# Optimization experiments

Hardware: AMD Instinct MI355X
Metric: run time of the kernel (lower is better)

The kernel has to match this reference:

```python
import jax, jax.numpy as jnp
import numpy as np

V = 33279   # num_tokens
E = 256     # embedding_size
H = 512     # hidden_size
NH = 8      # num_heads
L = 4       # num_layers
DH = E // NH
MAXPOS = 64


def _ln(x, g, b):
    mu = jnp.mean(x, axis=-1, keepdims=True)
    var = jnp.mean((x - mu) ** 2, axis=-1, keepdims=True)
    return (x - mu) / jnp.sqrt(var + 1e-5) * g + b


def setup_inputs() -> dict:
    key = jax.random.key(0)
    ks = jax.random.split(key, 32)
    N, S = 128, 64
    label = jax.random.randint(ks[0], (N, S), 0, V)
    # Bernoulli(0.15) BERT-style mask (deterministic stand-in for torch sampling)
    mask = (jax.random.uniform(ks[1], (N, S)) < 0.15).astype(jnp.int32)
    s = 0.02
    inp = {
        'label': label, 'mask': mask,
        'emb': jax.random.normal(ks[2], (V + 1, E)) * s,
        'pos': jax.random.normal(ks[3], (MAXPOS, E)) * s,
        'emb_g': jnp.ones((E,)), 'emb_b': jnp.zeros((E,)),
        # stacked per-layer params (leading dim L)
        'Wq': jax.random.normal(ks[4], (L, E, E)) * s, 'bq': jnp.zeros((L, E)),
        'Wk': jax.random.normal(ks[5], (L, E, E)) * s, 'bk': jnp.zeros((L, E)),
        'Wv': jax.random.normal(ks[6], (L, E, E)) * s, 'bv': jnp.zeros((L, E)),
        'Wo': jax.random.normal(ks[7], (L, E, E)) * s, 'bo': jnp.zeros((L, E)),
        'n1g': jnp.ones((L, E)), 'n1b': jnp.zeros((L, E)),
        'W1': jax.random.normal(ks[8], (L, E, H)) * s, 'b1': jnp.zeros((L, H)),
        'W2': jax.random.normal(ks[9], (L, H, E)) * s, 'b2': jnp.zeros((L, E)),
        'n2g': jnp.ones((L, E)), 'n2b': jnp.zeros((L, E)),
        # decoder head
        'dW1': jax.random.normal(ks[10], (E, E)) * s, 'db1': jnp.zeros((E,)),
        'dng': jnp.ones((E,)), 'dnb': jnp.zeros((E,)),
        'dW2': jax.random.normal(ks[11], (E, V)) * s, 'db2': jnp.zeros((V,)),
    }
    return inp


def reference(label, mask, emb, pos, emb_g, emb_b, Wq, bq, Wk, bk, Wv, bv,
              Wo, bo, n1g, n1b, W1, b1, W2, b2, n2g, n2b,
              dW1, db1, dng, dnb, dW2, db2):
    N, S = label.shape
    src_ids = jnp.where(mask == 1, V, label)  # masked-token id = num_tokens
    # embedding + positional, then LayerNorm (eval: Scaler/Dropout identity)
    x = emb[src_ids] + pos[:S][None, :, :]
    x = _ln(x, emb_g, emb_b)
    temp = jnp.asarray((E // NH) ** 0.5, x.dtype)

    def layer(x, p):
        wq, bq_, wk, bk_, wv, bv_, wo, bo_, g1, b1n, w1, b1_, w2, b2_, g2, b2n = p
        q = (x @ wq + bq_).reshape(N, S, NH, DH).transpose(0, 2, 1, 3)
        k = (x @ wk + bk_).reshape(N, S, NH, DH).transpose(0, 2, 1, 3)
        v = (x @ wv + bv_).reshape(N, S, NH, DH).transpose(0, 2, 1, 3)
        scores = jnp.einsum('nhsd,nhtd->nhst', q, k) / temp
        attn = jax.nn.softmax(scores, axis=-1)
        o = jnp.einsum('nhst,nhtd->nhsd', attn, v)
        o = o.transpose(0, 2, 1, 3).reshape(N, S, E) @ wo + bo_
        x1 = _ln(x + o, g1, b1n)
        ff = jax.nn.gelu(x1 @ w1 + b1_, approximate=False) @ w2 + b2_
        x2 = _ln(x1 + ff, g2, b2n)
        return x2, None

    x, _ = jax.lax.scan(layer, x, (Wq, bq, Wk, bk, Wv, bv, Wo, bo,
                                   n1g, n1b, W1, b1, W2, b2, n2g, n2b))
    # decoder head: linear -> gelu -> LN -> vocab projection
    h = jax.nn.gelu(x @ dW1 + db1, approximate=False)
    h = _ln(h, dng, dnb)
    logits = h @ dW2 + db2               # [N, S, V]
    logp = jax.nn.log_softmax(logits, axis=-1)
    loss = -jnp.take_along_axis(logp, label[..., None], axis=-1).mean()
    score = logits.transpose(0, 2, 1)    # [N, V, S] like torch permute(0,2,1)
    return score, loss
```

## Files before the change

kernel.cpp:

```cpp
#include <hip/hip_runtime.h>
#include <hip/hip_bf16.h>

#define DEVFN static __device__ __forceinline__

constexpr int N_ = 128, S_ = 64, T_ = N_ * S_;
constexpr int E_ = 256, H_ = 512, NH_ = 8, DH_ = 32, L_ = 4;
constexpr int V_ = 33279, VPAD_ = 33280, NVT_ = VPAD_ / 256;

typedef __attribute__((ext_vector_type(8))) short bf16x8;
typedef __attribute__((ext_vector_type(4))) float f32x4;
typedef unsigned short ushort_t;

DEVFN ushort_t f2bf(float f) {
  unsigned int u = __float_as_uint(f);
  unsigned int r = (u + 0x7fffu + ((u >> 16) & 1u)) >> 16;
  return (ushort_t)r;
}
DEVFN float bf2f(ushort_t u) { return __uint_as_float(((unsigned)u) << 16); }

DEVFN float geluf(float x) {
  return 0.5f * x * (1.f + erff(x * 0.70710678118654752440f));
}

DEVFN float wave_sum(float v) {
  #pragma unroll
  for (int off = 32; off >= 1; off >>= 1) v += __shfl_xor(v, off, 64);
  return v;
}

DEVFN float l15_sum(float v) {
  v += __shfl_xor(v, 1, 64);
  v += __shfl_xor(v, 2, 64);
  v += __shfl_xor(v, 4, 64);
  v += __shfl_xor(v, 8, 64);
  return v;
}

__global__ __launch_bounds__(256) void k_embed_ln(
    const int* __restrict__ label, const int* __restrict__ mask,
    const float* __restrict__ emb, const float* __restrict__ pos,
    const float* __restrict__ g, const float* __restrict__ b,
    float* __restrict__ x, ushort_t* __restrict__ xb) {
  int wv = threadIdx.x >> 6, lane = threadIdx.x & 63;
  int t = blockIdx.x * 4 + wv;
  int s = t & (S_ - 1);
  int id = (mask[t] == 1) ? V_ : label[t];
  int c = lane * 4;
  float4 v = *(const float4*)&emb[(size_t)id * E_ + c];
  float4 p = *(const float4*)&pos[s * E_ + c];
  v.x += p.x; v.y += p.y; v.z += p.z; v.w += p.w;
  float mean = wave_sum(v.x + v.y + v.z + v.w) * (1.f / E_);
  float4 d = {v.x - mean, v.y - mean, v.z - mean, v.w - mean};
  float var = wave_sum(d.x * d.x + d.y * d.y + d.z * d.z + d.w * d.w) * (1.f / E_);
  float rstd = 1.f / sqrtf(var + 1e-5f);
  float4 g4 = *(const float4*)&g[c];
  float4 b4 = *(const float4*)&b[c];
  float4 y = {d.x * rstd * g4.x + b4.x, d.y * rstd * g4.y + b4.y,
              d.z * rstd * g4.z + b4.z, d.w * rstd * g4.w + b4.w};
  *(float4*)&x[(size_t)t * E_ + c] = y;
  ushort4 yb = {f2bf(y.x), f2bf(y.y), f2bf(y.z), f2bf(y.w)};
  *(ushort4*)&xb[(size_t)t * E_ + c] = yb;
}

__global__ __launch_bounds__(256) void k_bcat(
    const float* __restrict__ bq, const float* __restrict__ bk,
    const float* __restrict__ bv, float* __restrict__ bqkv) {
  int l = blockIdx.x, i = threadIdx.x;
  bqkv[l * 768 + i]       = bq[l * 256 + i];
  bqkv[l * 768 + 256 + i] = bk[l * 256 + i];
  bqkv[l * 768 + 512 + i] = bv[l * 256 + i];
}

__global__ __launch_bounds__(256) void k_wt(const float* __restrict__ src,
                                            ushort_t* __restrict__ dst,
                                            int K, int J, int dstLayerStride) {
  __shared__ float tile[32][33];
  int j0 = blockIdx.x * 32, k0 = blockIdx.y * 32, l = blockIdx.z;
  src += (size_t)l * K * J;
  dst += (size_t)l * dstLayerStride;
  int tx = threadIdx.x & 31, ty = threadIdx.x >> 5;
  #pragma unroll
  for (int rr = 0; rr < 4; rr++) {
    int kk = ty * 4 + rr;
    tile[kk][tx] = src[(size_t)(k0 + kk) * J + j0 + tx];
  }
  __syncthreads();
  #pragma unroll
  for (int rr = 0; rr < 4; rr++) {
    int jj = ty * 4 + rr;
    dst[(size_t)(j0 + jj) * K + k0 + tx] = f2bf(tile[tx][jj]);
  }
}

__global__ __launch_bounds__(256) void k_wtE(
    const float* __restrict__ Wq, const float* __restrict__ Wk,
    const float* __restrict__ Wv, const float* __restrict__ Wo,
    const float* __restrict__ dW1, ushort_t* __restrict__ wqkvT,
    ushort_t* __restrict__ woT, ushort_t* __restrict__ dw1T) {
  __shared__ float tile[32][33];
  int z = blockIdx.z;
  const float* src;
  ushort_t* dst;
  if (z == 4 * L_) {
    src = dW1; dst = dw1T;
  } else {
    int w = z >> 2, l = z & 3;
    const float* ws = (w == 0) ? Wq : (w == 1) ? Wk : (w == 2) ? Wv : Wo;
    src = ws + (size_t)l * E_ * E_;
    dst = (w < 3) ? (wqkvT + (size_t)l * 768 * E_ + (size_t)w * 256 * E_)
                  : (woT + (size_t)l * E_ * E_);
  }
  int j0 = blockIdx.x * 32, k0 = blockIdx.y * 32;
  int tx = threadIdx.x & 31, ty = threadIdx.x >> 5;
  #pragma unroll
  for (int rr = 0; rr < 4; rr++) {
    int kk = ty * 4 + rr;
    tile[kk][tx] = src[(size_t)(k0 + kk) * E_ + j0 + tx];
  }
  __syncthreads();
  #pragma unroll
  for (int rr = 0; rr < 4; rr++) {
    int jj = ty * 4 + rr;
    dst[(size_t)(j0 + jj) * E_ + k0 + tx] = f2bf(tile[tx][jj]);
  }
}

template <int K, int OUT_BF16, int GELU_>
__global__ __launch_bounds__(256) void k_mm(
    const ushort_t* __restrict__ Xb, const ushort_t* __restrict__ WT,
    const float* __restrict__ bias, void* __restrict__ C, int Nout) {
  constexpr int STR = K + 8;
  __shared__ ushort_t xs[64 * STR];
  int tid = threadIdx.x, lane = tid & 63, wv = tid >> 6;
  int t0 = blockIdx.x * 64, j0 = blockIdx.y * 64;
  const ushort_t* xsrc = Xb + (size_t)t0 * K;
  for (int i = tid; i < 64 * (K / 8); i += 256) {
    int r = i / (K / 8), c = (i % (K / 8)) * 8;
    *(uint4*)&xs[r * STR + c] = *(const uint4*)&xsrc[(size_t)r * K + c];
  }
  __syncthreads();
  int l15 = lane & 15, l4 = lane >> 4;
  f32x4 acc[4] = {};
  const ushort_t* xrow = &xs[(wv * 16 + l15) * STR + l4 * 8];
  const ushort_t* wrow = WT + (size_t)j0 * K + l4 * 8;
  #pragma unroll
  for (int kb = 0; kb < K / 32; kb++) {
    bf16x8 a = *(const bf16x8*)(xrow + kb * 32);
    #pragma unroll
    for (int st = 0; st < 4; st++) {
      bf16x8 bfr = *(const bf16x8*)(wrow + (size_t)(st * 16 + l15) * K + kb * 32);
      acc[st] = __builtin_amdgcn_mfma_f32_16x16x32_bf16(a, bfr, acc[st], 0, 0, 0);
    }
  }
  #pragma unroll
  for (int st = 0; st < 4; st++) {
    int j = j0 + st * 16 + l15;
    float bv_ = bias[j];
    #pragma unroll
    for (int r = 0; r < 4; r++) {
      float val = acc[st][r] + bv_;
      if (GELU_) val = geluf(val);
      int t = t0 + wv * 16 + l4 * 4 + r;
      if (OUT_BF16)
        ((ushort_t*)C)[(size_t)t * Nout + j] = f2bf(val);
      else
        ((float*)C)[(size_t)t * Nout + j] = val;
    }
  }
}

template <int K, int GELU_PRE, int HAS_RES, int OUT_F32>
__global__ __launch_bounds__(256) void k_mm_ln2(
    const ushort_t* __restrict__ Xb, const ushort_t* __restrict__ WT,
    const float* __restrict__ bias, const float* __restrict__ res,
    const float* __restrict__ g, const float* __restrict__ bet,
    float* __restrict__ y, ushort_t* __restrict__ yb) {
  constexpr int STR = K + 8;
  __shared__ ushort_t xs[16 * STR];
  __shared__ float redA[4][16], redB[4][16];
  int tid = threadIdx.x, lane = tid & 63, wv = tid >> 6;
  int t0 = blockIdx.x * 16;
  const ushort_t* xsrc = Xb + (size_t)t0 * K;
  for (int i = tid; i < 16 * (K / 8); i += 256) {
    int r = i / (K / 8), c = (i % (K / 8)) * 8;
    *(uint4*)&xs[r * STR + c] = *(const uint4*)&xsrc[(size_t)r * K + c];
  }
  __syncthreads();
  int l15 = lane & 15, l4 = lane >> 4;
  f32x4 acc[4] = {};
  const ushort_t* xrow = &xs[l15 * STR + l4 * 8];
  const ushort_t* wrow = WT + (size_t)(wv * 64) * K + l4 * 8;
  #pragma unroll
  for (int kb = 0; kb < K / 32; kb++) {
    bf16x8 a = *(const bf16x8*)(xrow + kb * 32);
    #pragma unroll
    for (int st = 0; st < 4; st++) {
      bf16x8 bfr = *(const bf16x8*)(wrow + (size_t)(st * 16 + l15) * K + kb * 32);
      acc[st] = __builtin_amdgcn_mfma_f32_16x16x32_bf16(a, bfr, acc[st], 0, 0, 0);
    }
  }
  float val[4][4];
  #pragma unroll
  for (int st = 0; st < 4; st++) {
    int j = wv * 64 + st * 16 + l15;
    float bv_ = bias[j];
    #pragma unroll
    for (int r = 0; r < 4; r++) {
      float v = acc[st][r] + bv_;
      if (GELU_PRE) v = geluf(v);
      if (HAS_RES) v += res[(size_t)(t0 + l4 * 4 + r) * E_ + j];
      val[st][r] = v;
    }
  }
  #pragma unroll
  for (int r = 0; r < 4; r++) {
    float s = val[0][r] + val[1][r] + val[2][r] + val[3][r];
    s = l15_sum(s);
    if (l15 == 0) redA[wv][l4 * 4 + r] = s;
  }
  __syncthreads();
  float mean[4];
  #pragma unroll
  for (int r = 0; r < 4; r++) {
    int row = l4 * 4 + r;
    mean[r] = (redA[0][row] + redA[1][row] + redA[2][row] + redA[3][row]) * (1.f / E_);
  }
  #pragma unroll
  for (int r = 0; r < 4; r++) {
    float s = 0.f;
    #pragma unroll
    for (int st = 0; st < 4; st++) {
      float d = val[st][r] - mean[r];
      s += d * d;
    }
    s = l15_sum(s);
    if (l15 == 0) redB[wv][l4 * 4 + r] = s;
  }
  __syncthreads();
  float rstd[4];
  #pragma unroll
  for (int r = 0; r < 4; r++) {
    int row = l4 * 4 + r;
    float var = (redB[0][row] + redB[1][row] + redB[2][row] + redB[3][row]) * (1.f / E_);
    rstd[r] = 1.f / sqrtf(var + 1e-5f);
  }
  #pragma unroll
  for (int st = 0; st < 4; st++) {
    int j = wv * 64 + st * 16 + l15;
    float gj = g[j], bj = bet[j];
    #pragma unroll
    for (int r = 0; r < 4; r++) {
      int t = t0 + l4 * 4 + r;
      float o = (val[st][r] - mean[r]) * rstd[r] * gj + bj;
      if (OUT_F32) y[(size_t)t * E_ + j] = o;
      yb[(size_t)t * E_ + j] = f2bf(o);
    }
  }
}

__global__ __launch_bounds__(256) void k_attn(
    const ushort_t* __restrict__ qkv, ushort_t* __restrict__ o) {
  __shared__ __align__(16) ushort_t vt_[32 * 72];
  __shared__ __align__(16) ushort_t ps[64 * 72];
  int n = blockIdx.x >> 3, h = blockIdx.x & 7;
  int tid = threadIdx.x, lane = tid & 63, wv = tid >> 6;
  int l15 = lane & 15, l4 = lane >> 4;
  const ushort_t* qbase = qkv + (size_t)n * S_ * 768 + h * DH_;
  for (int i = tid; i < S_ * DH_; i += 256) {
    int t = i >> 5, d = i & 31;
    vt_[d * 72 + t] = qbase[(size_t)t * 768 + 512 + d];
  }
  int srow = wv * 16 + l15;
  bf16x8 aq = *(const bf16x8*)&qbase[(size_t)srow * 768 + l4 * 8];
  f32x4 sc[4];
  #pragma unroll
  for (int st = 0; st < 4; st++) {
    bf16x8 bk_ = *(const bf16x8*)&qbase[(size_t)(st * 16 + l15) * 768 + 256 + l4 * 8];
    f32x4 z = {};
    sc[st] = __builtin_amdgcn_mfma_f32_16x16x32_bf16(aq, bk_, z, 0, 0, 0);
  }
  const float scale = 0.17677669529663687f;
  #pragma unroll
  for (int st = 0; st < 4; st++)
    #pragma unroll
    for (int r = 0; r < 4; r++) sc[st][r] *= scale;
  #pragma unroll
  for (int r = 0; r < 4; r++) {
    float m = fmaxf(fmaxf(sc[0][r], sc[1][r]), fmaxf(sc[2][r], sc[3][r]));
    m = fmaxf(m, __shfl_xor(m, 1, 64));
    m = fmaxf(m, __shfl_xor(m, 2, 64));
    m = fmaxf(m, __shfl_xor(m, 4, 64));
    m = fmaxf(m, __shfl_xor(m, 8, 64));
    float p0 = __expf(sc[0][r] - m), p1 = __expf(sc[1][r] - m);
    float p2 = __expf(sc[2][r] - m), p3 = __expf(sc[3][r] - m);
    float sum = p0 + p1 + p2 + p3;
    sum += __shfl_xor(sum, 1, 64);
    sum += __shfl_xor(sum, 2, 64);
    sum += __shfl_xor(sum, 4, 64);
    sum += __shfl_xor(sum, 8, 64);
    float inv = 1.f / sum;
    int prow = (wv * 16 + l4 * 4 + r) * 72;
    ps[prow + 0 * 16 + l15] = f2bf(p0 * inv);
    ps[prow + 1 * 16 + l15] = f2bf(p1 * inv);
    ps[prow + 2 * 16 + l15] = f2bf(p2 * inv);
    ps[prow + 3 * 16 + l15] = f2bf(p3 * inv);
  }
  __syncthreads();
  f32x4 oc[2] = {};
  #pragma unroll
  for (int kb = 0; kb < 2; kb++) {
    bf16x8 ap = *(const bf16x8*)&ps[srow * 72 + kb * 32 + l4 * 8];
    #pragma unroll
    for (int st2 = 0; st2 < 2; st2++) {
      bf16x8 bv_ = *(const bf16x8*)&vt_[(st2 * 16 + l15) * 72 + kb * 32 + l4 * 8];
      oc[st2] = __builtin_amdgcn_mfma_f32_16x16x32_bf16(ap, bv_, oc[st2], 0, 0, 0);
    }
  }
  ushort_t* ob = o + (size_t)n * S_ * E_ + h * DH_;
  #pragma unroll
  for (int st2 = 0; st2 < 2; st2++)
    #pragma unroll
    for (int r = 0; r < 4; r++)
      ob[(size_t)(wv * 16 + l4 * 4 + r) * E_ + st2 * 16 + l15] = f2bf(oc[st2][r]);
}

__global__ __launch_bounds__(256) void k_w2t(const float* __restrict__ w,
                                             ushort_t* __restrict__ wt) {
  __shared__ float tile[32 * 33];
  int tx = threadIdx.x & 31, ty = threadIdx.x >> 5;
  int v0 = blockIdx.x * 32, k0 = blockIdx.y * 32;
  #pragma unroll
  for (int rr = 0; rr < 4; rr++) {
    int kk = ty * 4 + rr;
    int vv = v0 + tx;
    tile[kk * 33 + tx] = (vv < V_) ? w[(size_t)(k0 + kk) * V_ + vv] : 0.f;
  }
  __syncthreads();
  #pragma unroll
  for (int rr = 0; rr < 4; rr++) {
    int vv = ty * 4 + rr;
    wt[(size_t)(v0 + vv) * E_ + k0 + tx] = f2bf(tile[tx * 33 + vv]);
  }
}

__global__ __launch_bounds__(256) void k_vocab(
    const ushort_t* __restrict__ hbf, const ushort_t* __restrict__ wt,
    const float* __restrict__ db2, float* __restrict__ out,
    float* __restrict__ pmax, float* __restrict__ psum) {
  __shared__ ushort_t hs[64 * 264];
  __shared__ float redm[4][64];
  __shared__ float reds[4][64];
  int n = blockIdx.x, vt = blockIdx.y;
  int tid = threadIdx.x, lane = tid & 63, wv = tid >> 6;
  const ushort_t* hsrc = hbf + (size_t)n * S_ * E_;
  for (int i = tid; i < (S_ * E_) / 8; i += 256) {
    int s = i >> 5, kc = (i & 31) * 8;
    *(uint4*)&hs[s * 264 + kc] = *(const uint4*)&hsrc[s * E_ + kc];
  }
  __syncthreads();
  int l15 = lane & 15, l4 = lane >> 4;
  float rm[4], rs[4];
  #pragma unroll
  for (int st = 0; st < 4; st++) { rm[st] = -INFINITY; rs[st] = 0.f; }
  #pragma unroll
  for (int h2 = 0; h2 < 2; h2++) {
    const ushort_t* Ap0 =
        wt + (size_t)(vt * 256 + h2 * 128 + wv * 16 + l15) * E_ + l4 * 8;
    const ushort_t* Ap1 = Ap0 + (size_t)64 * E_;
    f32x4 acc[2][4] = {};
    #pragma unroll
    for (int kb = 0; kb < 8; kb++) {
      bf16x8 a0 = *(const bf16x8*)(Ap0 + kb * 32);
      bf16x8 a1 = *(const bf16x8*)(Ap1 + kb * 32);
      #pragma unroll
      for (int st = 0; st < 4; st++) {
        bf16x8 bfr = *(const bf16x8*)&hs[(st * 16 + l15) * 264 + kb * 32 + l4 * 8];
        acc[0][st] = __builtin_amdgcn_mfma_f32_16x16x32_bf16(a0, bfr, acc[0][st], 0, 0, 0);
        acc[1][st] = __builtin_amdgcn_mfma_f32_16x16x32_bf16(a1, bfr, acc[1][st], 0, 0, 0);
      }
    }
    float vals[2][4][4];
    #pragma unroll
    for (int mt = 0; mt < 2; mt++) {
      #pragma unroll
      for (int j = 0; j < 4; j++) {
        int v = vt * 256 + h2 * 128 + wv * 16 + mt * 64 + l4 * 4 + j;
        bool valid = v < V_;
        float bias = valid ? db2[v] : 0.f;
        size_t ob = ((size_t)n * V_ + v) * S_;
        #pragma unroll
        for (int st = 0; st < 4; st++) {
          float val = valid ? (acc[mt][st][j] + bias) : -INFINITY;
          vals[mt][st][j] = val;
          if (valid) __builtin_nontemporal_store(val, &out[ob + st * 16 + l15]);
        }
      }
    }
    #pragma unroll
    for (int st = 0; st < 4; st++) {
      float m = -INFINITY;
      #pragma unroll
      for (int mt = 0; mt < 2; mt++)
        #pragma unroll
        for (int j = 0; j < 4; j++) m = fmaxf(m, vals[mt][st][j]);
      m = fmaxf(m, __shfl_xor(m, 16, 64));
      m = fmaxf(m, __shfl_xor(m, 32, 64));
      float sum = 0.f;
      #pragma unroll
      for (int mt = 0; mt < 2; mt++)
        #pragma unroll
        for (int j = 0; j < 4; j++) sum += __expf(vals[mt][st][j] - m);
      sum += __shfl_xor(sum, 16, 64);
      sum += __shfl_xor(sum, 32, 64);
      float nm = fmaxf(rm[st], m);
      rs[st] = rs[st] * __expf(rm[st] - nm) + sum * __expf(m - nm);
      rm[st] = nm;
    }
  }
  if (l4 == 0) {
    #pragma unroll
    for (int st = 0; st < 4; st++) {
      redm[wv][st * 16 + l15] = rm[st];
      reds[wv][st * 16 + l15] = rs[st];
    }
  }
  __syncthreads();
  if (wv == 0 && l4 == 0) {
    #pragma unroll
    for (int st = 0; st < 4; st++) {
      int s = st * 16 + l15;
      float M = fmaxf(fmaxf(redm[0][s], redm[1][s]), fmaxf(redm[2][s], redm[3][s]));
      float Sa = reds[0][s] * __expf(redm[0][s] - M) +
                 reds[1][s] * __expf(redm[1][s] - M) +
                 reds[2][s] * __expf(redm[2][s] - M) +
                 reds[3][s] * __expf(redm[3][s] - M);
      size_t pi = ((size_t)n * NVT_ + vt) * S_ + s;
      pmax[pi] = M;
      psum[pi] = Sa;
    }
  }
}

__global__ __launch_bounds__(512) void k_lossf(
    const float* __restrict__ pmax, const float* __restrict__ psum,
    const float* __restrict__ out, const int* __restrict__ label,
    float* __restrict__ partial) {
  __shared__ float sm[512], ssum[512];
  int n = blockIdx.x, tid = threadIdx.x;
  int s = tid & 63, qq = tid >> 6;
  float m = -INFINITY, sum = 0.f;
  for (int vt = qq; vt < NVT_; vt += 8) {
    size_t pi = ((size_t)n * NVT_ + vt) * S_ + s;
    float m2 = pmax[pi], s2 = psum[pi];
    float nm = fmaxf(m, m2);
    sum = sum * __expf(m - nm) + s2 * __expf(m2 - nm);
    m = nm;
  }
  sm[tid] = m; ssum[tid] = sum;
  __syncthreads();
  if (qq == 0) {
    float M = sm[s], Sa = ssum[s];
    #pragma unroll
    for (int p = 1; p < 8; p++) {
      float m2 = sm[p * 64 + s], s2 = ssum[p * 64 + s];
      float nm = fmaxf(M, m2);
      Sa = Sa * __expf(M - nm) + s2 * __expf(m2 - nm);
      M = nm;
    }
    float lse = M + logf(Sa);
    int lab = label[n * S_ + s];
    float lx = out[((size_t)n * V_ + lab) * S_ + s];
    partial[n * S_ + s] = lse - lx;
  }
}

__global__ __launch_bounds__(256) void k_loss2(const float* __restrict__ partial,
                                               float* __restrict__ dst) {
  __shared__ float sbuf[4];
  int tid = threadIdx.x;
  float acc = 0.f;
  for (int i = tid; i < T_; i += 256) acc += partial[i];
  #pragma unroll
  for (int off = 32; off >= 1; off >>= 1) acc += __shfl_xor(acc, off, 64);
  int lane = tid & 63, wid = tid >> 6;
  if (lane == 0) sbuf[wid] = acc;
  __syncthreads();
  if (tid == 0) dst[0] = (sbuf[0] + sbuf[1] + sbuf[2] + sbuf[3]) / (float)T_;
}

extern "C" void kernel_launch(void* const* d_in, const int* in_sizes, int n_in,
                              void* d_out, int out_size, void* d_ws, size_t ws_size,
                              hipStream_t stream) {
  const int*   label = (const int*)d_in[0];
  const int*   mask  = (const int*)d_in[1];
  const float* emb   = (const float*)d_in[2];
  const float* pos   = (const float*)d_in[3];
  const float* emb_g = (const float*)d_in[4];
  const float* emb_b = (const float*)d_in[5];
  const float* Wq  = (const float*)d_in[6];
  const float* bq  = (const float*)d_in[7];
  const float* Wk  = (const float*)d_in[8];
  const float* bk  = (const float*)d_in[9];
  const float* Wv  = (const float*)d_in[10];
  const float* bv  = (const float*)d_in[11];
  const float* Wo  = (const float*)d_in[12];
  const float* bo  = (const float*)d_in[13];
  const float* n1g = (const float*)d_in[14];
  const float* n1b = (const float*)d_in[15];
  const float* W1  = (const float*)d_in[16];
  const float* b1  = (const float*)d_in[17];
  const float* W2  = (const float*)d_in[18];
  const float* b2  = (const float*)d_in[19];
  const float* n2g = (const float*)d_in[20];
  const float* n2b = (const float*)d_in[21];
  const float* dW1 = (const float*)d_in[22];
  const float* db1 = (const float*)d_in[23];
  const float* dng = (const float*)d_in[24];
  const float* dnb = (const float*)d_in[25];
  const float* dW2 = (const float*)d_in[26];
  const float* db2 = (const float*)d_in[27];
  float* out = (float*)d_out;
  (void)in_sizes; (void)n_in; (void)out_size; (void)ws_size;

  char* base = (char*)d_ws;
  size_t off = 0;
  auto alloc = [&](size_t bytes) {
    char* p = base + off;
    off += (bytes + 255) & ~(size_t)255;
    return p;
  };
  float*    x    = (float*)alloc((size_t)T_ * E_ * 4);
  ushort_t* xb   = (ushort_t*)alloc((size_t)T_ * E_ * 2);
  float*    x1   = (float*)alloc((size_t)T_ * E_ * 4);
  ushort_t* x1b  = (ushort_t*)alloc((size_t)T_ * E_ * 2);
  ushort_t* qkv  = (ushort_t*)alloc((size_t)T_ * 768 * 2);
  ushort_t* obuf = (ushort_t*)alloc((size_t)T_ * E_ * 2);
  ushort_t* wqkvT = (ushort_t*)alloc((size_t)L_ * 768 * E_ * 2);
  ushort_t* woT   = (ushort_t*)alloc((size_t)L_ * E_ * E_ * 2);
  ushort_t* w1T   = (ushort_t*)alloc((size_t)L_ * H_ * E_ * 2);
  ushort_t* w2T   = (ushort_t*)alloc((size_t)L_ * E_ * H_ * 2);
  ushort_t* dw1T  = (ushort_t*)alloc((size_t)E_ * E_ * 2);
  ushort_t* wt    = (ushort_t*)alloc((size_t)VPAD_ * E_ * 2);
  float*    bqkv  = (float*)alloc((size_t)L_ * 768 * 4);
  float*    partial = (float*)alloc((size_t)T_ * 4);
  ushort_t* ffh = qkv;
  ushort_t* hbf = obuf;
  float* pmax = x;
  float* psum = pmax + (size_t)N_ * NVT_ * S_;

  k_bcat<<<L_, 256, 0, stream>>>(bq, bk, bv, bqkv);
  k_wtE<<<dim3(8, 8, 4 * L_ + 1), 256, 0, stream>>>(Wq, Wk, Wv, Wo, dW1, wqkvT, woT, dw1T);
  k_wt<<<dim3(16, 8, L_), 256, 0, stream>>>(W1, w1T, E_, H_, H_ * E_);
  k_wt<<<dim3(8, 16, L_), 256, 0, stream>>>(W2, w2T, H_, E_, E_ * H_);
  k_w2t<<<dim3(VPAD_ / 32, E_ / 32), 256, 0, stream>>>(dW2, wt);

  k_embed_ln<<<T_ / 4, 256, 0, stream>>>(label, mask, emb, pos, emb_g, emb_b, x, xb);

  for (int l = 0; l < L_; l++) {
    k_mm<E_, 1, 0><<<dim3(T_ / 64, 12), 256, 0, stream>>>(
        xb, wqkvT + (size_t)l * 768 * E_, bqkv + l * 768, qkv, 768);
    k_attn<<<N_ * NH_, 256, 0, stream>>>(qkv, obuf);
    k_mm_ln2<E_, 0, 1, 1><<<T_ / 16, 256, 0, stream>>>(
        obuf, woT + (size_t)l * E_ * E_, bo + l * E_, x,
        n1g + l * E_, n1b + l * E_, x1, x1b);
    k_mm<E_, 1, 1><<<dim3(T_ / 64, 8), 256, 0, stream>>>(
        x1b, w1T + (size_t)l * H_ * E_, b1 + l * H_, ffh, H_);
    k_mm_ln2<H_, 0, 1, 1><<<T_ / 16, 256, 0, stream>>>(
        ffh, w2T + (size_t)l * E_ * H_, b2 + l * E_, x1,
        n2g + l * E_, n2b + l * E_, x, xb);
  }

  k_mm_ln2<E_, 1, 0, 0><<<T_ / 16, 256, 0, stream>>>(
      xb, dw1T, db1, nullptr, dng, dnb, nullptr, hbf);

  k_vocab<<<dim3(N_, NVT_), 256, 0, stream>>>(hbf, wt, db2, out, pmax, psum);

  k_lossf<<<N_, 512, 0, stream>>>(pmax, psum, out, label, partial);
  k_loss2<<<1, 256, 0, stream>>>(partial, out + (size_t)N_ * V_ * S_);
}
```

Measured before the change: 875.6 us.

## Fuse FFN up-projection, GELU, down-projection and LayerNorm into one kernel

Replaces the separate W1 GEMM (which wrote the GELU hidden to global memory) and the W2+residual+LN kernel with a single k_ff kernel. Each block handles 16 tokens and keeps the 512-wide hidden activation in shared memory. It also merges the four weight-prep launches into one k_prep kernel. This removes the global round trip of the FFN hidden tensor and a few launches per layer. The cost is lower weight reuse, since each 16-row block reads the full W1 and W2 from global/L2, and fewer rows per block for the first GEMM.

Measured after the change: 850.1 us. 1.03x faster.

```diff
diff --git a/kernel.cpp b/kernel.cpp
--- a/kernel.cpp
+++ b/kernel.cpp
@@ -62,22 +62,53 @@
   *(ushort4*)&xb[(size_t)t * E_ + c] = yb;
 }
 
-__global__ __launch_bounds__(256) void k_bcat(
-    const float* __restrict__ bq, const float* __restrict__ bk,
-    const float* __restrict__ bv, float* __restrict__ bqkv) {
-  int l = blockIdx.x, i = threadIdx.x;
-  bqkv[l * 768 + i]       = bq[l * 256 + i];
-  bqkv[l * 768 + 256 + i] = bk[l * 256 + i];
-  bqkv[l * 768 + 512 + i] = bv[l * 256 + i];
-}
-
-__global__ __launch_bounds__(256) void k_wt(const float* __restrict__ src,
-                                            ushort_t* __restrict__ dst,
-                                            int K, int J, int dstLayerStride) {
+__global__ __launch_bounds__(256) void k_prep(
+    const float* __restrict__ Wq, const float* __restrict__ Wk,
+    const float* __restrict__ Wv, const float* __restrict__ Wo,
+    const float* __restrict__ dW1, const float* __restrict__ W1,
+    const float* __restrict__ W2, const float* __restrict__ bq,
+    const float* __restrict__ bk, const float* __restrict__ bv,
+    ushort_t* __restrict__ wqkvT, ushort_t* __restrict__ woT,
+    ushort_t* __restrict__ dw1T, ushort_t* __restrict__ w1T,
+    ushort_t* __restrict__ w2T, float* __restrict__ bqkv) {
+  int z = blockIdx.z;
+  if (z == 25) {
+    if (blockIdx.x == 0 && blockIdx.y == 0) {
+      for (int i = threadIdx.x; i < L_ * 768; i += 256) {
+        int l = i / 768, c = i - l * 768;
+        float v = (c < 256) ? bq[l * 256 + c]
+                : (c < 512) ? bk[l * 256 + c - 256]
+                            : bv[l * 256 + c - 512];
+        bqkv[i] = v;
+      }
+    }
+    return;
+  }
+  const float* src;
+  ushort_t* dst;
+  int K, J;
+  if (z < 17) {
+    if (blockIdx.x >= 8 || blockIdx.y >= 8) return;
+    K = 256; J = 256;
+    if (z == 16) { src = dW1; dst = dw1T; }
+    else {
+      int w = z >> 2, l = z & 3;
+      const float* ws = (w == 0) ? Wq : (w == 1) ? Wk : (w == 2) ? Wv : Wo;
+      src = ws + (size_t)l * 65536;
+      dst = (w < 3) ? (wqkvT + (size_t)l * 768 * 256 + (size_t)w * 256 * 256)
+                    : (woT + (size_t)l * 65536);
+    }
+  } else if (z < 21) {
+    int l = z - 17; K = 256; J = 512;
+    if (blockIdx.y >= 8) return;
+    src = W1 + (size_t)l * K * J; dst = w1T + (size_t)l * J * K;
+  } else {
+    int l = z - 21; K = 512; J = 256;
+    if (blockIdx.x >= 8) return;
+    src = W2 + (size_t)l * K * J; dst = w2T + (size_t)l * J * K;
+  }
   __shared__ float tile[32][33];
-  int j0 = blockIdx.x * 32, k0 = blockIdx.y * 32, l = blockIdx.z;
-  src += (size_t)l * K * J;
-  dst += (size_t)l * dstLayerStride;
+  int j0 = blockIdx.x * 32, k0 = blockIdx.y * 32;
   int tx = threadIdx.x & 31, ty = threadIdx.x >> 5;
   #pragma unroll
   for (int rr = 0; rr < 4; rr++) {
@@ -89,39 +120,6 @@
   for (int rr = 0; rr < 4; rr++) {
     int jj = ty * 4 + rr;
     dst[(size_t)(j0 + jj) * K + k0 + tx] = f2bf(tile[tx][jj]);
-  }
-}
-
-__global__ __launch_bounds__(256) void k_wtE(
-    const float* __restrict__ Wq, const float* __restrict__ Wk,
-    const float* __restrict__ Wv, const float* __restrict__ Wo,
-    const float* __restrict__ dW1, ushort_t* __restrict__ wqkvT,
-    ushort_t* __restrict__ woT, ushort_t* __restrict__ dw1T) {
-  __shared__ float tile[32][33];
-  int z = blockIdx.z;
-  const float* src;
-  ushort_t* dst;
-  if (z == 4 * L_) {
-    src = dW1; dst = dw1T;
-  } else {
-    int w = z >> 2, l = z & 3;
-    const float* ws = (w == 0) ? Wq : (w == 1) ? Wk : (w == 2) ? Wv : Wo;
-    src = ws + (size_t)l * E_ * E_;
-    dst = (w < 3) ? (wqkvT + (size_t)l * 768 * E_ + (size_t)w * 256 * E_)
-                  : (woT + (size_t)l * E_ * E_);
-  }
-  int j0 = blockIdx.x * 32, k0 = blockIdx.y * 32;
-  int tx = threadIdx.x & 31, ty = threadIdx.x >> 5;
-  #pragma unroll
-  for (int rr = 0; rr < 4; rr++) {
-    int kk = ty * 4 + rr;
-    tile[kk][tx] = src[(size_t)(k0 + kk) * E_ + j0 + tx];
-  }
-  __syncthreads();
-  #pragma unroll
-  for (int rr = 0; rr < 4; rr++) {
-    int jj = ty * 4 + rr;
-    dst[(size_t)(j0 + jj) * E_ + k0 + tx] = f2bf(tile[tx][jj]);
   }
 }
 
@@ -253,6 +251,114 @@
       int t = t0 + l4 * 4 + r;
       float o = (val[st][r] - mean[r]) * rstd[r] * gj + bj;
       if (OUT_F32) y[(size_t)t * E_ + j] = o;
+      yb[(size_t)t * E_ + j] = f2bf(o);
+    }
+  }
+}
+
+__global__ __launch_bounds__(256) void k_ff(
+    const ushort_t* __restrict__ Xb, const ushort_t* __restrict__ W1T,
+    const float* __restrict__ b1v, const ushort_t* __restrict__ W2T,
+    const float* __restrict__ b2v, const float* __restrict__ res,
+    const float* __restrict__ g, const float* __restrict__ bet,
+    float* __restrict__ y, ushort_t* __restrict__ yb) {
+  __shared__ ushort_t xs[16 * 264];
+  __shared__ ushort_t hsd[16 * 520];
+  __shared__ float redA[4][16], redB[4][16];
+  int tid = threadIdx.x, lane = tid & 63, wv = tid >> 6;
+  int t0 = blockIdx.x * 16;
+  const ushort_t* xsrc = Xb + (size_t)t0 * E_;
+  for (int i = tid; i < 16 * 32; i += 256) {
+    int r = i >> 5, c = (i & 31) * 8;
+    *(uint4*)&xs[r * 264 + c] = *(const uint4*)&xsrc[(size_t)r * E_ + c];
+  }
+  __syncthreads();
+  int l15 = lane & 15, l4 = lane >> 4;
+  f32x4 acc1[8] = {};
+  const ushort_t* xrow = &xs[l15 * 264 + l4 * 8];
+  const ushort_t* w1r = W1T + (size_t)(wv * 128) * E_ + l4 * 8;
+  #pragma unroll
+  for (int kb = 0; kb < 8; kb++) {
+    bf16x8 a = *(const bf16x8*)(xrow + kb * 32);
+    #pragma unroll
+    for (int ht = 0; ht < 8; ht++) {
+      bf16x8 b = *(const bf16x8*)(w1r + (size_t)(ht * 16 + l15) * E_ + kb * 32);
+      acc1[ht] = __builtin_amdgcn_mfma_f32_16x16x32_bf16(a, b, acc1[ht], 0, 0, 0);
+    }
+  }
+  #pragma unroll
+  for (int ht = 0; ht < 8; ht++) {
+    int hc = wv * 128 + ht * 16 + l15;
+    float bv_ = b1v[hc];
+    #pragma unroll
+    for (int r = 0; r < 4; r++) {
+      float v = geluf(acc1[ht][r] + bv_);
+      hsd[(l4 * 4 + r) * 520 + hc] = f2bf(v);
+    }
+  }
+  __syncthreads();
+  f32x4 acc2[4] = {};
+  const ushort_t* hrow = &hsd[l15 * 520 + l4 * 8];
+  const ushort_t* w2r = W2T + (size_t)(wv * 64) * H_ + l4 * 8;
+  #pragma unroll
+  for (int kb = 0; kb < 16; kb++) {
+    bf16x8 a = *(const bf16x8*)(hrow + kb * 32);
+    #pragma unroll
+    for (int st = 0; st < 4; st++) {
+      bf16x8 b = *(const bf16x8*)(w2r + (size_t)(st * 16 + l15) * H_ + kb * 32);
+      acc2[st] = __builtin_amdgcn_mfma_f32_16x16x32_bf16(a, b, acc2[st], 0, 0, 0);
+    }
+  }
+  float val[4][4];
+  #pragma unroll
+  for (int st = 0; st < 4; st++) {
+    int j = wv * 64 + st * 16 + l15;
+    float bv_ = b2v[j];
+    #pragma unroll
+    for (int r = 0; r < 4; r++)
+      val[st][r] = acc2[st][r] + bv_ + res[(size_t)(t0 + l4 * 4 + r) * E_ + j];
+  }
+  #pragma unroll
+  for (int r = 0; r < 4; r++) {
+    float s = val[0][r] + val[1][r] + val[2][r] + val[3][r];
+    s = l15_sum(s);
+    if (l15 == 0) redA[wv][l4 * 4 + r] = s;
+  }
+  __syncthreads();
+  float mean[4];
+  #pragma unroll
+  for (int r = 0; r < 4; r++) {
+    int row = l4 * 4 + r;
+    mean[r] = (redA[0][row] + redA[1][row] + redA[2][row] + redA[3][row]) * (1.f / E_);
+  }
+  #pragma unroll
+  for (int r = 0; r < 4; r++) {
+    float s = 0.f;
+    #pragma unroll
+    for (int st = 0; st < 4; st++) {
+      float d = val[st][r] - mean[r];
+      s += d * d;
+    }
+    s = l15_sum(s);
+    if (l15 == 0) redB[wv][l4 * 4 + r] = s;
+  }
+  __syncthreads();
+  float rstd[4];
+  #pragma unroll
+  for (int r = 0; r < 4; r++) {
+    int row = l4 * 4 + r;
+    float var = (redB[0][row] + redB[1][row] + redB[2][row] + redB[3][row]) * (1.f / E_);
+    rstd[r] = 1.f / sqrtf(var + 1e-5f);
+  }
+  #pragma unroll
+  for (int st = 0; st < 4; st++) {
+    int j = wv * 64 + st * 16 + l15;
+    float gj = g[j], bj = bet[j];
+    #pragma unroll
+    for (int r = 0; r < 4; r++) {
+      int t = t0 + l4 * 4 + r;
+      float o = (val[st][r] - mean[r]) * rstd[r] * gj + bj;
+      y[(size_t)t * E_ + j] = o;
       yb[(size_t)t * E_ + j] = f2bf(o);
     }
   }
@@ -543,15 +649,13 @@
   ushort_t* wt    = (ushort_t*)alloc((size_t)VPAD_ * E_ * 2);
   float*    bqkv  = (float*)alloc((size_t)L_ * 768 * 4);
   float*    partial = (float*)alloc((size_t)T_ * 4);
-  ushort_t* ffh = qkv;
   ushort_t* hbf = obuf;
   float* pmax = x;
   float* psum = pmax + (size_t)N_ * NVT_ * S_;
 
-  k_bcat<<<L_, 256, 0, stream>>>(bq, bk, bv, bqkv);
-  k_wtE<<<dim3(8, 8, 4 * L_ + 1), 256, 0, stream>>>(Wq, Wk, Wv, Wo, dW1, wqkvT, woT, dw1T);
-  k_wt<<<dim3(16, 8, L_), 256, 0, stream>>>(W1, w1T, E_, H_, H_ * E_);
-  k_wt<<<dim3(8, 16, L_), 256, 0, stream>>>(W2, w2T, H_, E_, E_ * H_);
+  k_prep<<<dim3(16, 16, 26), 256, 0, stream>>>(Wq, Wk, Wv, Wo, dW1, W1, W2,
+                                               bq, bk, bv, wqkvT, woT, dw1T,
+                                               w1T, w2T, bqkv);
   k_w2t<<<dim3(VPAD_ / 32, E_ / 32), 256, 0, stream>>>(dW2, wt);
 
   k_embed_ln<<<T_ / 4, 256, 0, stream>>>(label, mask, emb, pos, emb_g, emb_b, x, xb);
@@ -563,10 +667,9 @@
     k_mm_ln2<E_, 0, 1, 1><<<T_ / 16, 256, 0, stream>>>(
         obuf, woT + (size_t)l * E_ * E_, bo + l * E_, x,
         n1g + l * E_, n1b + l * E_, x1, x1b);
-    k_mm<E_, 1, 1><<<dim3(T_ / 64, 8), 256, 0, stream>>>(
-        x1b, w1T + (size_t)l * H_ * E_, b1 + l * H_, ffh, H_);
-    k_mm_ln2<H_, 0, 1, 1><<<T_ / 16, 256, 0, stream>>>(
-        ffh, w2T + (size_t)l * E_ * H_, b2 + l * E_, x1,
+    k_ff<<<T_ / 16, 256, 0, stream>>>(
+        x1b, w1T + (size_t)l * H_ * E_, b1 + l * H_,
+        w2T + (size_t)l * E_ * H_, b2 + l * E_, x1,
         n2g + l * E_, n2b + l * E_, x, xb);
   }
 
```
